# Kernel tuning notes

Measured on AMD Instinct MI355X. Metric: run time of the kernel, lower is better.

Reference implementation:

```python
import jax, jax.numpy as jnp
import numpy as np

B, T, N, K, d = 16, 64, 256, 8, 8
D = K * d
NEG = -9e15  # matches torch's -9000000000000000.0 sentinel


def _xavier(key, out_dim, in_dim):
    lim = float(np.sqrt(6.0 / (in_dim + out_dim)))
    return jax.random.uniform(key, (out_dim, in_dim), jnp.float32, -lim, lim)


def setup_inputs() -> dict:
    key = jax.random.key(0)
    ks = jax.random.split(key, 12)
    X = jax.random.normal(ks[0], (B, T, N, D), jnp.float32)
    STE = jax.random.normal(ks[1], (B, T, N, D), jnp.float32)
    W12 = _xavier(ks[2], D, 2 * D); b12 = jnp.zeros((D,), jnp.float32)
    W13 = _xavier(ks[3], D, 2 * D); b13 = jnp.zeros((D,), jnp.float32)
    W14 = _xavier(ks[4], D, 2 * D); b14 = jnp.zeros((D,), jnp.float32)
    W15 = _xavier(ks[5], D, D);     b15 = jnp.zeros((D,), jnp.float32)
    W16 = _xavier(ks[6], D, D);     b16 = jnp.zeros((D,), jnp.float32)
    return dict(X=X, STE=STE, W12=W12, b12=b12, W13=W13, b13=b13,
                W14=W14, b14=b14, W15=W15, b15=b15, W16=W16, b16=b16)


def reference(X, STE, W12, b12, W13, b13, W14, b14, W15, b15, W16, b16):
    gelu = lambda x: jax.nn.gelu(x, approximate=False)  # torch F.gelu default = erf
    Bv, Tv, Nv, Dv = X.shape
    H = jnp.concatenate([X, STE], axis=-1)              # [B,T,N,2D]
    # GELU-activated QKV projections, split into K heads of width d on last dim
    q = gelu(H @ W12.T + b12).reshape(Bv, Tv, Nv, K, d)
    k = gelu(H @ W13.T + b13).reshape(Bv, Tv, Nv, K, d)
    v = gelu(H @ W14.T + b14).reshape(Bv, Tv, Nv, K, d)
    # attention over time axis per (batch, vertex, head)
    attn = jnp.einsum('bqnkd,bsnkd->bnkqs', q, k) / jnp.sqrt(jnp.float32(d))
    causal = jnp.tril(jnp.ones((Tv, Tv), bool))         # [T,T]
    attn = jnp.where(causal, attn, jnp.float32(NEG))
    attn = jax.nn.softmax(attn, axis=-1)
    out = jnp.einsum('bnkqs,bsnkd->bqnkd', attn, v).reshape(Bv, Tv, Nv, Dv)
    # output MLP (dropout is identity in eval)
    return gelu(out @ W15.T + b15) @ W16.T + b16
```

## Files before the change

kernel.cpp:

```cpp
#include <hip/hip_runtime.h>
#include <hip/hip_bf16.h>

#define Bn 16
#define Tn 64
#define Nn 256
#define Kn 8
#define dn 8
#define Dn 64
#define TDn 128

typedef __bf16 bf16x8 __attribute__((ext_vector_type(8)));
typedef __bf16 bf16x4 __attribute__((ext_vector_type(4)));
typedef float  f32x4  __attribute__((ext_vector_type(4)));
typedef float  f32x16 __attribute__((ext_vector_type(16)));

#if __has_builtin(__builtin_amdgcn_exp2f)
#define EXP2F(x) __builtin_amdgcn_exp2f(x)
#else
#define EXP2F(x) exp2f(x)
#endif

#if __has_builtin(__builtin_amdgcn_rcpf)
#define RCPF(x) __builtin_amdgcn_rcpf(x)
#else
#define RCPF(x) (1.0f / (x))
#endif

__device__ __forceinline__ float geluf(float x) {
    const float x2 = x * x;
    const float v = x * fmaf(0.10294342f, x2, 2.30220920f);
    const float w = EXP2F(-fabsf(v));
    const float r = RCPF(1.0f + w);
    const float t = (1.0f - w) * r;
    return fmaf(0.5f * fabsf(x), t, 0.5f * x);
}

__device__ __forceinline__ bf16x8 bzero8() {
    bf16x8 z;
    #pragma unroll
    for (int e = 0; e < 8; ++e) z[e] = (__bf16)0.0f;
    return z;
}

__device__ __forceinline__ bf16x8 pack8(float4 f0, float4 f1) {
    bf16x8 a;
    a[0] = (__bf16)f0.x; a[1] = (__bf16)f0.y;
    a[2] = (__bf16)f0.z; a[3] = (__bf16)f0.w;
    a[4] = (__bf16)f1.x; a[5] = (__bf16)f1.y;
    a[6] = (__bf16)f1.z; a[7] = (__bf16)f1.w;
    return a;
}

__device__ __forceinline__ char* ldsp(char* base, int row, int col) {
    return base + (((row << 7) + (col << 1)) ^ ((row & 7) << 4));
}

__global__ void convert_weights(const float* __restrict__ W12, const float* __restrict__ W13,
                                const float* __restrict__ W14, const float* __restrict__ W15,
                                const float* __restrict__ W16, __bf16* __restrict__ ws)
{
    const int i = blockIdx.x * 256 + threadIdx.x;
    float v;
    if      (i < 8192)  v = W12[i];
    else if (i < 16384) v = W13[i - 8192];
    else if (i < 24576) v = W14[i - 16384];
    else if (i < 28672) v = W15[i - 24576];
    else                v = W16[i - 28672];
    ws[i] = (__bf16)v;
}

__global__ __launch_bounds__(256, 3)
void tam_fused(const float* __restrict__ X,
               const float* __restrict__ STE,
               const float* __restrict__ b12, const float* __restrict__ b13,
               const float* __restrict__ b14, const float* __restrict__ b15,
               const float* __restrict__ b16,
               const __bf16* __restrict__ Wb,
               float* __restrict__ Out)
{
    __shared__ __align__(16) char smem[49152];
    char* const vtb[2] = { smem,         smem + 24576 };
    char* const qsb[2] = { smem + 8192,  smem + 24576 + 8192 };
    char* const ksb[2] = { smem + 16384, smem + 24576 + 16384 };

    const int bn   = blockIdx.x;
    const int b    = bn >> 7;
    const int n0   = (bn & 127) * 2;
    const int tid  = threadIdx.x;
    const int lane = tid & 63;
    const int wv   = __builtin_amdgcn_readfirstlane(tid >> 6);
    const int cl   = lane & 15;
    const int quad = lane >> 4;
    const int kb   = quad * 8;
    const int m0   = wv * 16;

    const __bf16* Wqkv = Wb;
    const __bf16* W15b = Wb + 24576;
    const __bf16* W16b = Wb + 28672;

    {
        bf16x8 af[2][4];
        {
            const int t = m0 + cl;
            const size_t rb = (((size_t)b * Tn + t) * Nn + n0) * (size_t)Dn;
            #pragma unroll
            for (int c = 0; c < 2; ++c) {
                const float4* Xr = reinterpret_cast<const float4*>(X + rb + c * Dn);
                const float4* Sr = reinterpret_cast<const float4*>(STE + rb + c * Dn);
                const int fi = quad * 2;
                const float4 x0 = Xr[fi], x1 = Xr[fi + 1];
                const float4 x2 = Xr[8 + fi], x3 = Xr[8 + fi + 1];
                const float4 s0 = Sr[fi], s1 = Sr[fi + 1];
                const float4 s2 = Sr[8 + fi], s3 = Sr[8 + fi + 1];
                af[c][0] = pack8(x0, x1);
                af[c][1] = pack8(x2, x3);
                af[c][2] = pack8(s0, s1);
                af[c][3] = pack8(s2, s3);
            }
        }

        #pragma unroll
        for (int nt = 0; nt < 12; ++nt) {
            const int nf = nt * 16;
            bf16x8 wq[4];
            #pragma unroll
            for (int kk = 0; kk < 4; ++kk)
                wq[kk] = *reinterpret_cast<const bf16x8*>(&Wqkv[(nf + cl) * TDn + kk * 32 + kb]);
            f32x4 acc[2] = { {0.f, 0.f, 0.f, 0.f}, {0.f, 0.f, 0.f, 0.f} };
            if (nt < 8) {
                #pragma unroll
                for (int kk = 0; kk < 4; ++kk) {
                    #pragma unroll
                    for (int c = 0; c < 2; ++c)
                        acc[c] = __builtin_amdgcn_mfma_f32_16x16x32_bf16(wq[kk], af[c][kk], acc[c], 0, 0, 0);
                }
                if (nt < 4) {
                    const float4 bs = *reinterpret_cast<const float4*>(&b12[nf + 4 * quad]);
                    #pragma unroll
                    for (int c = 0; c < 2; ++c) {
                        bf16x4 pk;
                        pk[0] = (__bf16)(geluf(acc[c][0] + bs.x) * 0.51006951f);
                        pk[1] = (__bf16)(geluf(acc[c][1] + bs.y) * 0.51006951f);
                        pk[2] = (__bf16)(geluf(acc[c][2] + bs.z) * 0.51006951f);
                        pk[3] = (__bf16)(geluf(acc[c][3] + bs.w) * 0.51006951f);
                        *reinterpret_cast<bf16x4*>(ldsp(qsb[c], m0 + cl, nf + 4 * quad)) = pk;
                    }
                } else {
                    const float4 bs = *reinterpret_cast<const float4*>(&b13[nf - 64 + 4 * quad]);
                    #pragma unroll
                    for (int c = 0; c < 2; ++c) {
                        bf16x4 pk;
                        pk[0] = (__bf16)geluf(acc[c][0] + bs.x);
                        pk[1] = (__bf16)geluf(acc[c][1] + bs.y);
                        pk[2] = (__bf16)geluf(acc[c][2] + bs.z);
                        pk[3] = (__bf16)geluf(acc[c][3] + bs.w);
                        *reinterpret_cast<bf16x4*>(ldsp(ksb[c], m0 + cl, nf - 64 + 4 * quad)) = pk;
                    }
                }
            } else {
                #pragma unroll
                for (int kk = 0; kk < 4; ++kk) {
                    #pragma unroll
                    for (int c = 0; c < 2; ++c)
                        acc[c] = __builtin_amdgcn_mfma_f32_16x16x32_bf16(af[c][kk], wq[kk], acc[c], 0, 0, 0);
                }
                const float vbias = b14[nf - 128 + cl];
                #pragma unroll
                for (int c = 0; c < 2; ++c) {
                    bf16x4 pv;
                    #pragma unroll
                    for (int r = 0; r < 4; ++r) pv[r] = (__bf16)geluf(acc[c][r] + vbias);
                    *reinterpret_cast<bf16x4*>(ldsp(vtb[c], nf - 128 + cl, m0 + 4 * quad)) = pv;
                }
            }
        }
    }
    __syncthreads();

    {
        const int half = lane >> 5;
        const int l31  = lane & 31;

        for (int hh = 0; hh < 2; ++hh) {
            const int hc = 8 * (2 * wv + hh);

            bf16x8 kA0[2], kA1[2], qB0[2], qB1[2], vA0[2], vA1[2];
            #pragma unroll
            for (int c = 0; c < 2; ++c) {
                kA0[c] = bzero8(); kA1[c] = bzero8(); qB0[c] = bzero8(); qB1[c] = bzero8();
                vA0[c] = bzero8(); vA1[c] = bzero8();
                if (half == 0) {
                    kA0[c] = *reinterpret_cast<const bf16x8*>(ldsp(ksb[c],  0 + l31, hc));
                    kA1[c] = *reinterpret_cast<const bf16x8*>(ldsp(ksb[c], 32 + l31, hc));
                    qB0[c] = *reinterpret_cast<const bf16x8*>(ldsp(qsb[c],  0 + l31, hc));
                    qB1[c] = *reinterpret_cast<const bf16x8*>(ldsp(qsb[c], 32 + l31, hc));
                }
                if (l31 < 8) {
                    vA0[c] = *reinterpret_cast<const bf16x8*>(ldsp(vtb[c], hc + l31,  0 + 8 * half));
                    vA1[c] = *reinterpret_cast<const bf16x8*>(ldsp(vtb[c], hc + l31, 16 + 8 * half));
                }
            }

            f32x16 zc16;
            #pragma unroll
            for (int r = 0; r < 16; ++r) zc16[r] = 0.f;

            {
                f32x16 S[2];
                #pragma unroll
                for (int c = 0; c < 2; ++c)
                    S[c] = __builtin_amdgcn_mfma_f32_32x32x16_bf16(kA0[c], qB0[c], zc16, 0, 0, 0);
                #pragma unroll
                for (int r = 0; r < 16; ++r) {
                    const int tk = (r & 3) + 8 * (r >> 2) + 4 * half;
                    #pragma unroll
                    for (int c = 0; c < 2; ++c) S[c][r] = (tk > l31) ? -3.0e38f : S[c][r];
                }
                float mx[2] = { S[0][0], S[1][0] };
                #pragma unroll
                for (int r = 1; r < 16; ++r) {
                    #pragma unroll
                    for (int c = 0; c < 2; ++c) mx[c] = fmaxf(mx[c], S[c][r]);
                }
                #pragma unroll
                for (int c = 0; c < 2; ++c) mx[c] = fmaxf(mx[c], __shfl_xor(mx[c], 32));
                float sum[2] = { 0.f, 0.f };
                #pragma unroll
                for (int r = 0; r < 16; ++r) {
                    #pragma unroll
                    for (int c = 0; c < 2; ++c) {
                        const float p = EXP2F(S[c][r] - mx[c]);
                        S[c][r] = p; sum[c] += p;
                    }
                }
                #pragma unroll
                for (int c = 0; c < 2; ++c) sum[c] += __shfl_xor(sum[c], 32);

                unsigned u[2][8];
                #pragma unroll
                for (int i = 0; i < 8; ++i) {
                    #pragma unroll
                    for (int c = 0; c < 2; ++c) {
                        union { __bf16 h[2]; unsigned w; } cv;
                        cv.h[0] = (__bf16)S[c][2 * i]; cv.h[1] = (__bf16)S[c][2 * i + 1];
                        u[c][i] = cv.w;
                    }
                }
                f32x16 O[2] = { zc16, zc16 };
                #pragma unroll
                for (int ch = 0; ch < 2; ++ch) {
                    #pragma unroll
                    for (int c = 0; c < 2; ++c) {
                        const unsigned x0 = __shfl_xor(u[c][4 * ch + 0], 32);
                        const unsigned x1 = __shfl_xor(u[c][4 * ch + 1], 32);
                        const unsigned x2 = __shfl_xor(u[c][4 * ch + 2], 32);
                        const unsigned x3 = __shfl_xor(u[c][4 * ch + 3], 32);
                        union { unsigned w[4]; bf16x8 v; } bw;
                        bw.w[0] = half ? x2 : u[c][4 * ch + 0];
                        bw.w[1] = half ? x3 : u[c][4 * ch + 1];
                        bw.w[2] = half ? u[c][4 * ch + 2] : x0;
                        bw.w[3] = half ? u[c][4 * ch + 3] : x1;
                        O[c] = __builtin_amdgcn_mfma_f32_32x32x16_bf16(ch ? vA1[c] : vA0[c],
                                                                       bw.v, O[c], 0, 0, 0);
                    }
                }
                #pragma unroll
                for (int c = 0; c < 2; ++c) {
                    const float inv = RCPF(sum[c]);
                    bf16x4 ov;
                    #pragma unroll
                    for (int r = 0; r < 4; ++r) ov[r] = (__bf16)(O[c][r] * inv);
                    *reinterpret_cast<bf16x4*>(ldsp(qsb[c], l31, hc + 4 * half)) = ov;
                }
            }

            {
                bf16x8 vA2[2], vA3[2];
                #pragma unroll
                for (int c = 0; c < 2; ++c) {
                    vA2[c] = bzero8(); vA3[c] = bzero8();
                    if (l31 < 8) {
                        vA2[c] = *reinterpret_cast<const bf16x8*>(ldsp(vtb[c], hc + l31, 32 + 8 * half));
                        vA3[c] = *reinterpret_cast<const bf16x8*>(ldsp(vtb[c], hc + l31, 48 + 8 * half));
                    }
                }
                f32x16 Sa[2], Sb[2];
                #pragma unroll
                for (int c = 0; c < 2; ++c) {
                    Sa[c] = __builtin_amdgcn_mfma_f32_32x32x16_bf16(kA0[c], qB1[c], zc16, 0, 0, 0);
                    Sb[c] = __builtin_amdgcn_mfma_f32_32x32x16_bf16(kA1[c], qB1[c], zc16, 0, 0, 0);
                }
                #pragma unroll
                for (int r = 0; r < 16; ++r) {
                    const int tk = (r & 3) + 8 * (r >> 2) + 4 * half;
                    #pragma unroll
                    for (int c = 0; c < 2; ++c) Sb[c][r] = (tk > l31) ? -3.0e38f : Sb[c][r];
                }
                float mx[2] = { Sa[0][0], Sa[1][0] };
                #pragma unroll
                for (int r = 1; r < 16; ++r) {
                    #pragma unroll
                    for (int c = 0; c < 2; ++c) mx[c] = fmaxf(mx[c], Sa[c][r]);
                }
                #pragma unroll
                for (int r = 0; r < 16; ++r) {
                    #pragma unroll
                    for (int c = 0; c < 2; ++c) mx[c] = fmaxf(mx[c], Sb[c][r]);
                }
                #pragma unroll
                for (int c = 0; c < 2; ++c) mx[c] = fmaxf(mx[c], __shfl_xor(mx[c], 32));
                float sum[2] = { 0.f, 0.f };
                #pragma unroll
                for (int r = 0; r < 16; ++r) {
                    #pragma unroll
                    for (int c = 0; c < 2; ++c) {
                        const float p = EXP2F(Sa[c][r] - mx[c]); Sa[c][r] = p; sum[c] += p;
                    }
                }
                #pragma unroll
                for (int r = 0; r < 16; ++r) {
                    #pragma unroll
                    for (int c = 0; c < 2; ++c) {
                        const float p = EXP2F(Sb[c][r] - mx[c]); Sb[c][r] = p; sum[c] += p;
                    }
                }
                #pragma unroll
                for (int c = 0; c < 2; ++c) sum[c] += __shfl_xor(sum[c], 32);

                unsigned ua[2][8], ub[2][8];
                #pragma unroll
                for (int i = 0; i < 8; ++i) {
                    #pragma unroll
                    for (int c = 0; c < 2; ++c) {
                        union { __bf16 h[2]; unsigned w; } cv;
                        cv.h[0] = (__bf16)Sa[c][2 * i]; cv.h[1] = (__bf16)Sa[c][2 * i + 1];
                        ua[c][i] = cv.w;
                        union { __bf16 h[2]; unsigned w; } cw;
                        cw.h[0] = (__bf16)Sb[c][2 * i]; cw.h[1] = (__bf16)Sb[c][2 * i + 1];
                        ub[c][i] = cw.w;
                    }
                }
                f32x16 O[2] = { zc16, zc16 };
                #pragma unroll
                for (int ch = 0; ch < 4; ++ch) {
                    const int c2 = ch & 1;
                    #pragma unroll
                    for (int c = 0; c < 2; ++c) {
                        const unsigned* uu = (ch < 2) ? ua[c] : ub[c];
                        const unsigned x0 = __shfl_xor(uu[4 * c2 + 0], 32);
                        const unsigned x1 = __shfl_xor(uu[4 * c2 + 1], 32);
                        const unsigned x2 = __shfl_xor(uu[4 * c2 + 2], 32);
                        const unsigned x3 = __shfl_xor(uu[4 * c2 + 3], 32);
                        union { unsigned w[4]; bf16x8 v; } bw;
                        bw.w[0] = half ? x2 : uu[4 * c2 + 0];
                        bw.w[1] = half ? x3 : uu[4 * c2 + 1];
                        bw.w[2] = half ? uu[4 * c2 + 2] : x0;
                        bw.w[3] = half ? uu[4 * c2 + 3] : x1;
                        const bf16x8 vA = (ch == 0) ? vA0[c] : (ch == 1) ? vA1[c]
                                        : (ch == 2) ? vA2[c] : vA3[c];
                        O[c] = __builtin_amdgcn_mfma_f32_32x32x16_bf16(vA, bw.v, O[c], 0, 0, 0);
                    }
                }
                #pragma unroll
                for (int c = 0; c < 2; ++c) {
                    const float inv = RCPF(sum[c]);
                    bf16x4 ov;
                    #pragma unroll
                    for (int r = 0; r < 4; ++r) ov[r] = (__bf16)(O[c][r] * inv);
                    *reinterpret_cast<bf16x4*>(ldsp(qsb[c], 32 + l31, hc + 4 * half)) = ov;
                }
            }
        }
    }
    __syncthreads();

    {
        bf16x8 h0[2], h1[2];
        #pragma unroll
        for (int c = 0; c < 2; ++c) {
            h0[c] = *reinterpret_cast<const bf16x8*>(ldsp(qsb[c], m0 + cl, kb));
            h1[c] = *reinterpret_cast<const bf16x8*>(ldsp(qsb[c], m0 + cl, 32 + kb));
        }
        #pragma unroll
        for (int nt = 0; nt < 4; ++nt) {
            const int nf = nt * 16;
            const bf16x8 w0 = *reinterpret_cast<const bf16x8*>(&W15b[(nf + cl) * Dn + kb]);
            const bf16x8 w1 = *reinterpret_cast<const bf16x8*>(&W15b[(nf + cl) * Dn + 32 + kb]);
            const float4 bs = *reinterpret_cast<const float4*>(&b15[nf + 4 * quad]);
            #pragma unroll
            for (int c = 0; c < 2; ++c) {
                f32x4 acc = {0.f, 0.f, 0.f, 0.f};
                acc = __builtin_amdgcn_mfma_f32_16x16x32_bf16(w0, h0[c], acc, 0, 0, 0);
                acc = __builtin_amdgcn_mfma_f32_16x16x32_bf16(w1, h1[c], acc, 0, 0, 0);
                bf16x4 pk;
                pk[0] = (__bf16)geluf(acc[0] + bs.x);
                pk[1] = (__bf16)geluf(acc[1] + bs.y);
                pk[2] = (__bf16)geluf(acc[2] + bs.z);
                pk[3] = (__bf16)geluf(acc[3] + bs.w);
                *reinterpret_cast<bf16x4*>(ldsp(ksb[c], m0 + cl, nf + 4 * quad)) = pk;
            }
        }
        bf16x8 g0[2], g1[2];
        #pragma unroll
        for (int c = 0; c < 2; ++c) {
            g0[c] = *reinterpret_cast<const bf16x8*>(ldsp(ksb[c], m0 + cl, kb));
            g1[c] = *reinterpret_cast<const bf16x8*>(ldsp(ksb[c], m0 + cl, 32 + kb));
        }
        const size_t ob = (((size_t)(b * Tn + m0 + cl)) * Nn + n0) * (size_t)Dn;
        #pragma unroll
        for (int nt = 0; nt < 4; ++nt) {
            const int nf = nt * 16;
            const bf16x8 w0 = *reinterpret_cast<const bf16x8*>(&W16b[(nf + cl) * Dn + kb]);
            const bf16x8 w1 = *reinterpret_cast<const bf16x8*>(&W16b[(nf + cl) * Dn + 32 + kb]);
            const float4 bs = *reinterpret_cast<const float4*>(&b16[nf + 4 * quad]);
            #pragma unroll
            for (int c = 0; c < 2; ++c) {
                f32x4 acc = {0.f, 0.f, 0.f, 0.f};
                acc = __builtin_amdgcn_mfma_f32_16x16x32_bf16(w0, g0[c], acc, 0, 0, 0);
                acc = __builtin_amdgcn_mfma_f32_16x16x32_bf16(w1, g1[c], acc, 0, 0, 0);
                float4 ov;
                ov.x = acc[0] + bs.x;
                ov.y = acc[1] + bs.y;
                ov.z = acc[2] + bs.z;
                ov.w = acc[3] + bs.w;
                *reinterpret_cast<float4*>(&Out[ob + (size_t)c * Dn + nf + 4 * quad]) = ov;
            }
        }
    }
}

extern "C" void kernel_launch(void* const* d_in, const int* in_sizes, int n_in,
                              void* d_out, int out_size, void* d_ws, size_t ws_size,
                              hipStream_t stream)
{
    (void)in_sizes; (void)n_in; (void)out_size; (void)ws_size;
    const float* X   = (const float*)d_in[0];
    const float* STE = (const float*)d_in[1];
    const float* W12 = (const float*)d_in[2];
    const float* b12 = (const float*)d_in[3];
    const float* W13 = (const float*)d_in[4];
    const float* b13 = (const float*)d_in[5];
    const float* W14 = (const float*)d_in[6];
    const float* b14 = (const float*)d_in[7];
    const float* W15 = (const float*)d_in[8];
    const float* b15 = (const float*)d_in[9];
    const float* W16 = (const float*)d_in[10];
    const float* b16 = (const float*)d_in[11];
    float* Out = (float*)d_out;
    __bf16* ws = (__bf16*)d_ws;

    hipLaunchKernelGGL(convert_weights, dim3(128), dim3(256), 0, stream,
                       W12, W13, W14, W15, W16, ws);
    hipLaunchKernelGGL(tam_fused, dim3(Bn * Nn / 2), dim3(256), 0, stream,
                       X, STE, b12, b13, b14, b15, b16, ws, Out);
}
```

Baseline: 245.7 us.

## Partition QKV projection by feature columns per wave and drop the block barrier

Each wave now computes the Q, K and V projections for its own 16-feature slice across all 64 time steps. Previously each wave computed all 192 output features for 16 time rows. Because the attention stage only reads each wave's own head columns, the wave produces exactly what it consumes, so the __syncthreads between projection and attention is removed. Projection weights and biases are loaded once per wave instead of per tile. In exchange, every wave reloads the full X/STE tile, which quadruples cache-level input traffic per block.

```diff
diff --git a/kernel.cpp b/kernel.cpp
--- a/kernel.cpp
+++ b/kernel.cpp
@@ -93,89 +93,75 @@
     const int quad = lane >> 4;
     const int kb   = quad * 8;
     const int m0   = wv * 16;
+    const int fb   = wv * 16;
 
     const __bf16* Wqkv = Wb;
     const __bf16* W15b = Wb + 24576;
     const __bf16* W16b = Wb + 28672;
 
     {
-        bf16x8 af[2][4];
-        {
-            const int t = m0 + cl;
-            const size_t rb = (((size_t)b * Tn + t) * Nn + n0) * (size_t)Dn;
+        bf16x8 wqA[4], wkA[4], wvB[4];
+        #pragma unroll
+        for (int kk = 0; kk < 4; ++kk) {
+            wqA[kk] = *reinterpret_cast<const bf16x8*>(&Wqkv[(fb + cl) * TDn + kk * 32 + kb]);
+            wkA[kk] = *reinterpret_cast<const bf16x8*>(&Wqkv[(64 + fb + cl) * TDn + kk * 32 + kb]);
+            wvB[kk] = *reinterpret_cast<const bf16x8*>(&Wqkv[(128 + fb + cl) * TDn + kk * 32 + kb]);
+        }
+        const float4 bq = *reinterpret_cast<const float4*>(&b12[fb + 4 * quad]);
+        const float4 bk = *reinterpret_cast<const float4*>(&b13[fb + 4 * quad]);
+        const float  vb = b14[fb + cl];
+
+        #pragma unroll
+        for (int tt = 0; tt < 4; ++tt) {
+            bf16x8 hf[2][4];
+            {
+                const size_t rb = (((size_t)b * Tn + 16 * tt + cl) * Nn + n0) * (size_t)Dn;
+                #pragma unroll
+                for (int c = 0; c < 2; ++c) {
+                    const float4* Xr = reinterpret_cast<const float4*>(X + rb + c * Dn);
+                    const float4* Sr = reinterpret_cast<const float4*>(STE + rb + c * Dn);
+                    const int fi = quad * 2;
+                    hf[c][0] = pack8(Xr[fi],     Xr[fi + 1]);
+                    hf[c][1] = pack8(Xr[8 + fi], Xr[8 + fi + 1]);
+                    hf[c][2] = pack8(Sr[fi],     Sr[fi + 1]);
+                    hf[c][3] = pack8(Sr[8 + fi], Sr[8 + fi + 1]);
+                }
+            }
+            f32x4 qa[2] = { {0.f,0.f,0.f,0.f}, {0.f,0.f,0.f,0.f} };
+            f32x4 ka[2] = { {0.f,0.f,0.f,0.f}, {0.f,0.f,0.f,0.f} };
+            f32x4 va[2] = { {0.f,0.f,0.f,0.f}, {0.f,0.f,0.f,0.f} };
+            #pragma unroll
+            for (int kk = 0; kk < 4; ++kk) {
+                #pragma unroll
+                for (int c = 0; c < 2; ++c) {
+                    qa[c] = __builtin_amdgcn_mfma_f32_16x16x32_bf16(wqA[kk], hf[c][kk], qa[c], 0, 0, 0);
+                    ka[c] = __builtin_amdgcn_mfma_f32_16x16x32_bf16(wkA[kk], hf[c][kk], ka[c], 0, 0, 0);
+                    va[c] = __builtin_amdgcn_mfma_f32_16x16x32_bf16(hf[c][kk], wvB[kk], va[c], 0, 0, 0);
+                }
+            }
             #pragma unroll
             for (int c = 0; c < 2; ++c) {
-                const float4* Xr = reinterpret_cast<const float4*>(X + rb + c * Dn);
-                const float4* Sr = reinterpret_cast<const float4*>(STE + rb + c * Dn);
-                const int fi = quad * 2;
-                const float4 x0 = Xr[fi], x1 = Xr[fi + 1];
-                const float4 x2 = Xr[8 + fi], x3 = Xr[8 + fi + 1];
-                const float4 s0 = Sr[fi], s1 = Sr[fi + 1];
-                const float4 s2 = Sr[8 + fi], s3 = Sr[8 + fi + 1];
-                af[c][0] = pack8(x0, x1);
-                af[c][1] = pack8(x2, x3);
-                af[c][2] = pack8(s0, s1);
-                af[c][3] = pack8(s2, s3);
-            }
-        }
-
-        #pragma unroll
-        for (int nt = 0; nt < 12; ++nt) {
-            const int nf = nt * 16;
-            bf16x8 wq[4];
-            #pragma unroll
-            for (int kk = 0; kk < 4; ++kk)
-                wq[kk] = *reinterpret_cast<const bf16x8*>(&Wqkv[(nf + cl) * TDn + kk * 32 + kb]);
-            f32x4 acc[2] = { {0.f, 0.f, 0.f, 0.f}, {0.f, 0.f, 0.f, 0.f} };
-            if (nt < 8) {
-                #pragma unroll
-                for (int kk = 0; kk < 4; ++kk) {
-                    #pragma unroll
-                    for (int c = 0; c < 2; ++c)
-                        acc[c] = __builtin_amdgcn_mfma_f32_16x16x32_bf16(wq[kk], af[c][kk], acc[c], 0, 0, 0);
-                }
-                if (nt < 4) {
-                    const float4 bs = *reinterpret_cast<const float4*>(&b12[nf + 4 * quad]);
-                    #pragma unroll
-                    for (int c = 0; c < 2; ++c) {
-                        bf16x4 pk;
-                        pk[0] = (__bf16)(geluf(acc[c][0] + bs.x) * 0.51006951f);
-                        pk[1] = (__bf16)(geluf(acc[c][1] + bs.y) * 0.51006951f);
-                        pk[2] = (__bf16)(geluf(acc[c][2] + bs.z) * 0.51006951f);
-                        pk[3] = (__bf16)(geluf(acc[c][3] + bs.w) * 0.51006951f);
-                        *reinterpret_cast<bf16x4*>(ldsp(qsb[c], m0 + cl, nf + 4 * quad)) = pk;
-                    }
-                } else {
-                    const float4 bs = *reinterpret_cast<const float4*>(&b13[nf - 64 + 4 * quad]);
-                    #pragma unroll
-                    for (int c = 0; c < 2; ++c) {
-                        bf16x4 pk;
-                        pk[0] = (__bf16)geluf(acc[c][0] + bs.x);
-                        pk[1] = (__bf16)geluf(acc[c][1] + bs.y);
-                        pk[2] = (__bf16)geluf(acc[c][2] + bs.z);
-                        pk[3] = (__bf16)geluf(acc[c][3] + bs.w);
-                        *reinterpret_cast<bf16x4*>(ldsp(ksb[c], m0 + cl, nf - 64 + 4 * quad)) = pk;
-                    }
-                }
-            } else {
-                #pragma unroll
-                for (int kk = 0; kk < 4; ++kk) {
-                    #pragma unroll
-                    for (int c = 0; c < 2; ++c)
-                        acc[c] = __builtin_amdgcn_mfma_f32_16x16x32_bf16(af[c][kk], wq[kk], acc[c], 0, 0, 0);
-                }
-                const float vbias = b14[nf - 128 + cl];
-                #pragma unroll
-                for (int c = 0; c < 2; ++c) {
-                    bf16x4 pv;
-                    #pragma unroll
-                    for (int r = 0; r < 4; ++r) pv[r] = (__bf16)geluf(acc[c][r] + vbias);
-                    *reinterpret_cast<bf16x4*>(ldsp(vtb[c], nf - 128 + cl, m0 + 4 * quad)) = pv;
-                }
+                bf16x4 pq;
+                pq[0] = (__bf16)(geluf(qa[c][0] + bq.x) * 0.51006951f);
+                pq[1] = (__bf16)(geluf(qa[c][1] + bq.y) * 0.51006951f);
+                pq[2] = (__bf16)(geluf(qa[c][2] + bq.z) * 0.51006951f);
+                pq[3] = (__bf16)(geluf(qa[c][3] + bq.w) * 0.51006951f);
+                *reinterpret_cast<bf16x4*>(ldsp(qsb[c], 16 * tt + cl, fb + 4 * quad)) = pq;
+                bf16x4 pk;
+                pk[0] = (__bf16)geluf(ka[c][0] + bk.x);
+                pk[1] = (__bf16)geluf(ka[c][1] + bk.y);
+                pk[2] = (__bf16)geluf(ka[c][2] + bk.z);
+                pk[3] = (__bf16)geluf(ka[c][3] + bk.w);
+                *reinterpret_cast<bf16x4*>(ldsp(ksb[c], 16 * tt + cl, fb + 4 * quad)) = pk;
+                bf16x4 pv;
+                pv[0] = (__bf16)geluf(va[c][0] + vb);
+                pv[1] = (__bf16)geluf(va[c][1] + vb);
+                pv[2] = (__bf16)geluf(va[c][2] + vb);
+                pv[3] = (__bf16)geluf(va[c][3] + vb);
+                *reinterpret_cast<bf16x4*>(ldsp(vtb[c], fb + cl, 16 * tt + 4 * quad)) = pv;
             }
         }
     }
-    __syncthreads();
 
     {
         const int half = lane >> 5;
```

New measurement: 243.9 us. About the same (-0.7%).
